# Optimization experiments

Hardware: AMD Instinct MI355X
Metric: run time of the kernel (lower is better)

The kernel has to match this reference:

```python
import jax, jax.numpy as jnp
import numpy as np

D = 128; PATCH = 16; NE = 1024; BETA = 0.25; EPS = 1e-5

def _conv1d(x, w, b, stride=1, pad=(0, 0)):
    # x: [N, Cin, L], w: [Cout, Cin, K] (torch OIW layout)
    x = jnp.pad(x, ((0, 0), (0, 0), pad))
    y = jax.lax.conv_general_dilated(x, w, (stride,), 'VALID', dimension_numbers=('NCH', 'OIH', 'NCH'))
    return y + b[None, :, None]

def _causal(x, w, b):
    # Conv1d(padding=k-1) followed by Chomp1d(k-1) == left-pad-only causal conv
    return _conv1d(x, w, b, pad=(w.shape[-1] - 1, 0))

def _block(x, w1, b1, w2, b2, wd=None, bd=None):
    h = jax.nn.relu(_causal(x, w1, b1))
    h = jax.nn.relu(_causal(h, w2, b2))
    res = x if wd is None else _conv1d(x, wd, bd)
    return jax.nn.relu(h + res)

def _forward(x, revin_w, revin_b, tb0_w1, tb0_b1, tb0_w2, tb0_b2, tb0_wd, tb0_bd,
             tb1_w1, tb1_b1, tb1_w2, tb1_b2, proj_w, proj_b, embed,
             up_w, up_b, dec_w1, dec_b1, dec_w2, dec_b2):
    B, L, C = x.shape
    # channel-independent: [B, L, C] -> [B*C, L, 1]
    x = jnp.transpose(x, (0, 2, 1)).reshape(B * C, L, 1)
    # RevIN normalization over the time axis (affine, enc_in=1)
    mu = x.mean(axis=1, keepdims=True)
    var = x.var(axis=1, keepdims=True)
    x_norm = (x - mu) / jnp.sqrt(var + EPS) * revin_w + revin_b
    # TCN encoder on [B*C, 1, L]
    h = jnp.transpose(x_norm, (0, 2, 1))
    h = _block(h, tb0_w1, tb0_b1, tb0_w2, tb0_b2, tb0_wd, tb0_bd)
    h = _block(h, tb1_w1, tb1_b1, tb1_w2, tb1_b2)            # [B*C, D, L]
    # patchify: Conv1d(D, D, kernel=patch_len, stride=patch_len)
    pf = _conv1d(h, proj_w, proj_b, stride=PATCH)            # [B*C, D, P]
    pf = jnp.transpose(pf, (0, 2, 1))                        # [B*C, P, D]
    # Vector quantization (eval mode: no EMA buffer update)
    flat = pf.reshape(-1, D)                                 # [N, D]
    dist = (flat * flat).sum(1, keepdims=True) - 2.0 * (flat @ embed) + (embed * embed).sum(0, keepdims=True)
    ind = jnp.argmin(dist, axis=1)                           # [N]
    q = jnp.take(embed.T, ind, axis=0).reshape(pf.shape)     # [B*C, P, D]
    vq_loss = jnp.mean((jax.lax.stop_gradient(q) - pf) ** 2) * BETA
    z_q = pf + jax.lax.stop_gradient(q - pf)                 # straight-through
    # lightweight decoder: ConvTranspose1d(k=stride=patch_len) == per-patch expansion
    z = jnp.transpose(z_q, (0, 2, 1))                        # [B*C, D, P]
    up = jnp.einsum('bep,edj->bdpj', z, up_w).reshape(z.shape[0], up_w.shape[1], -1) + up_b[None, :, None]
    d = jax.nn.gelu(_conv1d(up, dec_w1, dec_b1, pad=(1, 1)), approximate=False)
    d = _conv1d(d, dec_w2, dec_b2, pad=(1, 1))
    dec_out = jnp.transpose(d, (0, 2, 1))                    # [B*C, L, 1]
    recon_loss = jnp.mean((dec_out - x_norm) ** 2)
    return z_q, recon_loss + vq_loss

def setup_inputs():
    key = jax.random.key(0)
    ks = jax.random.split(key, 24)
    n = lambda i, s: jax.random.normal(ks[i], s, jnp.float32)
    return {
        'x': n(0, (64, 1024, 8)),
        'revin_w': jnp.ones((1,), jnp.float32), 'revin_b': jnp.zeros((1,), jnp.float32),
        'tb0_w1': n(1, (D, 1, 3)) * 0.01, 'tb0_b1': n(2, (D,)) * 0.01,
        'tb0_w2': n(3, (D, D, 3)) * 0.01, 'tb0_b2': n(4, (D,)) * 0.01,
        'tb0_wd': n(5, (D, 1, 1)) * 0.01, 'tb0_bd': n(6, (D,)) * 0.01,
        'tb1_w1': n(7, (D, D, 3)) * 0.01, 'tb1_b1': n(8, (D,)) * 0.01,
        'tb1_w2': n(9, (D, D, 3)) * 0.01, 'tb1_b2': n(10, (D,)) * 0.01,
        'proj_w': n(11, (D, D, PATCH)) * 0.02, 'proj_b': n(12, (D,)) * 0.02,
        'embed': n(13, (D, NE)),
        'up_w': n(14, (D, D, PATCH)) * 0.02, 'up_b': n(15, (D,)) * 0.02,
        'dec_w1': n(16, (D // 2, D, 3)) * 0.05, 'dec_b1': n(17, (D // 2,)) * 0.05,
        'dec_w2': n(18, (1, D // 2, 3)) * 0.05, 'dec_b2': n(19, (1,)) * 0.05,
    }

def reference(x, revin_w, revin_b, tb0_w1, tb0_b1, tb0_w2, tb0_b2, tb0_wd, tb0_bd,
              tb1_w1, tb1_b1, tb1_w2, tb1_b2, proj_w, proj_b, embed,
              up_w, up_b, dec_w1, dec_b1, dec_w2, dec_b2):
    return _forward(x, revin_w, revin_b, tb0_w1, tb0_b1, tb0_w2, tb0_b2, tb0_wd, tb0_bd,
                    tb1_w1, tb1_b1, tb1_w2, tb1_b2, proj_w, proj_b, embed,
                    up_w, up_b, dec_w1, dec_b1, dec_w2, dec_b2)
```

## Files before the change

### kernel.cpp

```cpp
#include <hip/hip_runtime.h>

constexpr size_t OFF_XN  = 0;
constexpr size_t OFF_PF  = 524288;
constexpr size_t OFF_W2A = OFF_PF  + 4194304;
constexpr size_t OFF_W1B = OFF_W2A + 49152;
constexpr size_t OFF_W2B = OFF_W1B + 49152;
constexpr size_t OFF_PW  = OFF_W2B + 49152;
constexpr size_t OFF_UPW = OFF_PW  + 262144;
constexpr size_t OFF_W1D = OFF_UPW + 262144;
constexpr size_t OFF_EMT = OFF_W1D + 24576;
constexpr size_t OFF_EN  = OFF_EMT + 131072;
constexpr size_t OFF_RP  = OFF_EN  + 1024;
constexpr size_t OFF_VP  = OFF_RP  + 8192;
constexpr size_t OFF_IND = OFF_VP  + 4096;

#define DI __device__ __forceinline__

__global__ __launch_bounds__(256) void k_prep(
    const float* __restrict__ w2a, const float* __restrict__ w1b, const float* __restrict__ w2b,
    const float* __restrict__ pw,  const float* __restrict__ upw, const float* __restrict__ w1d,
    const float* __restrict__ em,  float* __restrict__ ws)
{
  int tid = blockIdx.x * 256 + threadIdx.x;
  int stride = gridDim.x * 256;
  for (int i = tid; i < 128*128*3; i += stride) {
    int d = i / 384, r = i % 384;
    ws[OFF_W2A + (size_t)r*128 + d] = w2a[i];
    ws[OFF_W1B + (size_t)r*128 + d] = w1b[i];
    ws[OFF_W2B + (size_t)r*128 + d] = w2b[i];
  }
  for (int i = tid; i < 128*128*16; i += stride) {
    int d = i / 2048, r = i % 2048;
    ws[OFF_PW + (size_t)r*128 + d] = pw[i];
  }
  for (int i = tid; i < 128*128*16; i += stride) {
    int e = i / 2048, rem = i % 2048;
    int d = rem / 16, j = rem % 16;
    ws[OFF_UPW + (size_t)(j*128 + e)*128 + d] = upw[i];
  }
  for (int i = tid; i < 64*128*3; i += stride) {
    int o = i / 384, r = i % 384;
    ws[OFF_W1D + (size_t)r*64 + o] = w1d[i];
  }
  for (int j = tid; j < 1024; j += stride) {
    float s = 0.f;
    for (int d = 0; d < 128; ++d) {
      float v = em[d*1024 + j];
      ws[OFF_EMT + (size_t)j*128 + d] = v;
      s = fmaf(v, v, s);
    }
    ws[OFF_EN + j] = s;
  }
}

__global__ __launch_bounds__(256) void k_revin(
    const float* __restrict__ x, const float* __restrict__ rw, const float* __restrict__ rb,
    float* __restrict__ xn)
{
  int n = blockIdx.x;
  int b = n >> 3, c = n & 7;
  int t = threadIdx.x;
  const float* xp = x + (size_t)b*8192 + c;
  float v[4]; float s = 0.f, s2 = 0.f;
  #pragma unroll
  for (int i = 0; i < 4; ++i) {
    v[i] = xp[(size_t)(t + i*256)*8];
    s += v[i]; s2 = fmaf(v[i], v[i], s2);
  }
  __shared__ float sh[8];
  __shared__ float st[2];
  for (int o = 32; o; o >>= 1) { s += __shfl_down(s, o, 64); s2 += __shfl_down(s2, o, 64); }
  if ((t & 63) == 0) { sh[t >> 6] = s; sh[4 + (t >> 6)] = s2; }
  __syncthreads();
  if (t == 0) {
    float S = sh[0]+sh[1]+sh[2]+sh[3];
    float S2 = sh[4]+sh[5]+sh[6]+sh[7];
    float mu = S * (1.f/1024.f);
    float var = S2 * (1.f/1024.f) - mu*mu;
    st[0] = mu;
    st[1] = 1.f / sqrtf(var + 1e-5f);
  }
  __syncthreads();
  float mu = st[0], inv = st[1], w0 = rw[0], b0 = rb[0];
  #pragma unroll
  for (int i = 0; i < 4; ++i)
    xn[(size_t)n*1024 + t + i*256] = fmaf((v[i]-mu)*inv, w0, b0);
}

constexpr int STA = 70;
constexpr int STB = 68;

__global__ __launch_bounds__(512) void k_enc(
    const float* __restrict__ xn, float* __restrict__ pf,
    const float* __restrict__ w1a, const float* __restrict__ b1a,
    const float* __restrict__ w2aT, const float* __restrict__ b2a,
    const float* __restrict__ wd,  const float* __restrict__ bd,
    const float* __restrict__ w1bT, const float* __restrict__ b1b,
    const float* __restrict__ w2bT, const float* __restrict__ b2b,
    const float* __restrict__ pwT, const float* __restrict__ pb)
{
  __shared__ float xs[72];
  __shared__ __align__(16) float bufA[64*STA];
  __shared__ __align__(16) float bufB[128*STB];
  int n = blockIdx.x >> 4, tile = blockIdx.x & 15;
  int l0 = tile * 64;
  int t = threadIdx.x;
  int lane = t & 63;
  int w = __builtin_amdgcn_readfirstlane(t >> 6);
  int d0 = w * 16;

  if (t < 72) {
    int gl = l0 - 8 + t;
    xs[t] = (gl >= 0) ? xn[(size_t)n*1024 + gl] : 0.f;
  }
  __syncthreads();

  float acc2[16];
  #pragma unroll
  for (int i = 0; i < 16; ++i) acc2[i] = 0.f;
  float hacc[4] = {0.f, 0.f, 0.f, 0.f};

  for (int rep = 0; rep < 2; ++rep) {
    {
      int row = t & 63, colg = t >> 6;
      int c = rep*64 + row;
      float w0 = w1a[c*3+0], w1 = w1a[c*3+1], w2 = w1a[c*3+2], bb = b1a[c];
      #pragma unroll
      for (int i = 0; i < 9; ++i) {
        int j = colg*9 + i;
        if (j < 70) {
          float v = fmaf(w0, xs[j], fmaf(w1, xs[j+1], fmaf(w2, xs[j+2], bb)));
          bufA[row*STA + j] = (l0 - 6 + j >= 0) ? fmaxf(v, 0.f) : 0.f;
        }
      }
    }
    __syncthreads();
    for (int cc2 = 0; cc2 < 64; ++cc2) {
      float r0 = bufA[cc2*STA + lane + 4];
      float r1 = bufA[cc2*STA + lane + 5];
      float r2 = bufA[cc2*STA + lane + 6];
      const float4* wp = (const float4*)(w2aT + (size_t)(rep*64 + cc2)*384 + d0);
      #pragma unroll
      for (int jj = 0; jj < 4; ++jj) {
        float4 a = wp[jj], b = wp[32+jj], c4 = wp[64+jj];
        acc2[jj*4+0] = fmaf(a.x, r0, fmaf(b.x, r1, fmaf(c4.x, r2, acc2[jj*4+0])));
        acc2[jj*4+1] = fmaf(a.y, r0, fmaf(b.y, r1, fmaf(c4.y, r2, acc2[jj*4+1])));
        acc2[jj*4+2] = fmaf(a.z, r0, fmaf(b.z, r1, fmaf(c4.z, r2, acc2[jj*4+2])));
        acc2[jj*4+3] = fmaf(a.w, r0, fmaf(b.w, r1, fmaf(c4.w, r2, acc2[jj*4+3])));
      }
    }
    if (t < 128) {
      for (int cc2 = 0; cc2 < 64; ++cc2) {
        const float* wp = w2aT + (size_t)(rep*64 + cc2)*384 + t;
        float w0 = wp[0], w1 = wp[128], w2 = wp[256];
        float q0 = bufA[cc2*STA+0], q1 = bufA[cc2*STA+1], q2 = bufA[cc2*STA+2],
              q3 = bufA[cc2*STA+3], q4 = bufA[cc2*STA+4], q5 = bufA[cc2*STA+5];
        hacc[0] = fmaf(w0, q0, fmaf(w1, q1, fmaf(w2, q2, hacc[0])));
        hacc[1] = fmaf(w0, q1, fmaf(w1, q2, fmaf(w2, q3, hacc[1])));
        hacc[2] = fmaf(w0, q2, fmaf(w1, q3, fmaf(w2, q4, hacc[2])));
        hacc[3] = fmaf(w0, q3, fmaf(w1, q4, fmaf(w2, q5, hacc[3])));
      }
    }
    __syncthreads();
  }

  {
    float xv = xs[lane + 8];
    #pragma unroll
    for (int i = 0; i < 16; ++i) {
      int d = d0 + i;
      bufB[d*STB + lane + 4] =
        fmaxf(fmaxf(acc2[i] + b2a[d], 0.f) + fmaf(wd[d], xv, bd[d]), 0.f);
    }
    if (t < 128) {
      #pragma unroll
      for (int h = 0; h < 4; ++h) {
        int l = l0 - 4 + h;
        float o = 0.f;
        if (l >= 0)
          o = fmaxf(fmaxf(hacc[h] + b2a[t], 0.f) + fmaf(wd[t], xs[h+4], bd[t]), 0.f);
        bufB[t*STB + h] = o;
      }
    }
  }
  __syncthreads();

  float acc4[16];
  #pragma unroll
  for (int i = 0; i < 16; ++i) acc4[i] = 0.f;
  for (int rep = 0; rep < 2; ++rep) {
    {
      float acc3[8];
      #pragma unroll
      for (int i = 0; i < 8; ++i) acc3[i] = 0.f;
      int dh = rep*64 + w*8;
      for (int cc = 0; cc < 128; ++cc) {
        float r0 = bufB[cc*STB + lane];
        float r1 = bufB[cc*STB + lane + 1];
        float r2 = bufB[cc*STB + lane + 2];
        const float4* wp = (const float4*)(w1bT + (size_t)cc*384 + dh);
        float4 a0 = wp[0],  a1 = wp[1];
        float4 b0 = wp[32], b1 = wp[33];
        float4 c0 = wp[64], c1 = wp[65];
        acc3[0] = fmaf(a0.x, r0, fmaf(b0.x, r1, fmaf(c0.x, r2, acc3[0])));
        acc3[1] = fmaf(a0.y, r0, fmaf(b0.y, r1, fmaf(c0.y, r2, acc3[1])));
        acc3[2] = fmaf(a0.z, r0, fmaf(b0.z, r1, fmaf(c0.z, r2, acc3[2])));
        acc3[3] = fmaf(a0.w, r0, fmaf(b0.w, r1, fmaf(c0.w, r2, acc3[3])));
        acc3[4] = fmaf(a1.x, r0, fmaf(b1.x, r1, fmaf(c1.x, r2, acc3[4])));
        acc3[5] = fmaf(a1.y, r0, fmaf(b1.y, r1, fmaf(c1.y, r2, acc3[5])));
        acc3[6] = fmaf(a1.z, r0, fmaf(b1.z, r1, fmaf(c1.z, r2, acc3[6])));
        acc3[7] = fmaf(a1.w, r0, fmaf(b1.w, r1, fmaf(c1.w, r2, acc3[7])));
      }
      bool valid = (l0 - 2 + lane >= 0);
      #pragma unroll
      for (int i = 0; i < 8; ++i)
        bufA[(w*8+i)*STA + lane] = valid ? fmaxf(acc3[i] + b1b[dh+i], 0.f) : 0.f;
      if (t < 64) {
        int d = rep*64 + t;
        float h0 = 0.f, h1v = 0.f;
        for (int cc = 0; cc < 128; ++cc) {
          const float* wp = w1bT + (size_t)cc*384 + d;
          float w0 = wp[0], w1 = wp[128], w2 = wp[256];
          float q0 = bufB[cc*STB + 64], q1 = bufB[cc*STB + 65],
                q2 = bufB[cc*STB + 66], q3 = bufB[cc*STB + 67];
          h0  = fmaf(w0, q0, fmaf(w1, q1, fmaf(w2, q2, h0)));
          h1v = fmaf(w0, q1, fmaf(w1, q2, fmaf(w2, q3, h1v)));
        }
        bufA[t*STA + 64] = fmaxf(h0  + b1b[d], 0.f);
        bufA[t*STA + 65] = fmaxf(h1v + b1b[d], 0.f);
      }
    }
    __syncthreads();
    for (int row = 0; row < 64; ++row) {
      float r0 = bufA[row*STA + lane];
      float r1 = bufA[row*STA + lane + 1];
      float r2 = bufA[row*STA + lane + 2];
      const float4* wp = (const float4*)(w2bT + (size_t)(rep*64 + row)*384 + d0);
      #pragma unroll
      for (int jj = 0; jj < 4; ++jj) {
        float4 a = wp[jj], b = wp[32+jj], c4 = wp[64+jj];
        acc4[jj*4+0] = fmaf(a.x, r0, fmaf(b.x, r1, fmaf(c4.x, r2, acc4[jj*4+0])));
        acc4[jj*4+1] = fmaf(a.y, r0, fmaf(b.y, r1, fmaf(c4.y, r2, acc4[jj*4+1])));
        acc4[jj*4+2] = fmaf(a.z, r0, fmaf(b.z, r1, fmaf(c4.z, r2, acc4[jj*4+2])));
        acc4[jj*4+3] = fmaf(a.w, r0, fmaf(b.w, r1, fmaf(c4.w, r2, acc4[jj*4+3])));
      }
    }
    __syncthreads();
  }

  {
    float o1[16];
    #pragma unroll
    for (int i = 0; i < 16; ++i) {
      float res = bufB[(d0+i)*STB + lane + 4];
      o1[i] = fmaxf(fmaxf(acc4[i] + b2b[d0+i], 0.f) + res, 0.f);
    }
    __syncthreads();
    #pragma unroll
    for (int i = 0; i < 16; ++i) bufB[(d0+i)*STB + lane] = o1[i];
  }
  __syncthreads();

  {
    int cq = t >> 7, dd = t & 127;
    float accp[4] = {0.f, 0.f, 0.f, 0.f};
    for (int cl = 0; cl < 32; ++cl) {
      int c = cq*32 + cl;
      const float* row = bufB + c*STB;
      const float* wrow = pwT + (size_t)c*2048 + dd;
      float wv[16];
      #pragma unroll
      for (int k = 0; k < 16; ++k) wv[k] = wrow[(size_t)k*128];
      #pragma unroll
      for (int p = 0; p < 4; ++p) {
        float4 a0 = *(const float4*)(row + p*16);
        float4 a1 = *(const float4*)(row + p*16 + 4);
        float4 a2 = *(const float4*)(row + p*16 + 8);
        float4 a3 = *(const float4*)(row + p*16 + 12);
        accp[p] = fmaf(a0.x, wv[0],  accp[p]);
        accp[p] = fmaf(a0.y, wv[1],  accp[p]);
        accp[p] = fmaf(a0.z, wv[2],  accp[p]);
        accp[p] = fmaf(a0.w, wv[3],  accp[p]);
        accp[p] = fmaf(a1.x, wv[4],  accp[p]);
        accp[p] = fmaf(a1.y, wv[5],  accp[p]);
        accp[p] = fmaf(a1.z, wv[6],  accp[p]);
        accp[p] = fmaf(a1.w, wv[7],  accp[p]);
        accp[p] = fmaf(a2.x, wv[8],  accp[p]);
        accp[p] = fmaf(a2.y, wv[9],  accp[p]);
        accp[p] = fmaf(a2.z, wv[10], accp[p]);
        accp[p] = fmaf(a2.w, wv[11], accp[p]);
        accp[p] = fmaf(a3.x, wv[12], accp[p]);
        accp[p] = fmaf(a3.y, wv[13], accp[p]);
        accp[p] = fmaf(a3.z, wv[14], accp[p]);
        accp[p] = fmaf(a3.w, wv[15], accp[p]);
      }
    }
    #pragma unroll
    for (int p = 0; p < 4; ++p) bufA[(cq*4 + p)*128 + dd] = accp[p];
  }
  __syncthreads();
  {
    int p = t >> 7, dd = t & 127;
    float s = bufA[p*128 + dd];
    s += bufA[(4 + p)*128 + dd];
    s += bufA[(8 + p)*128 + dd];
    s += bufA[(12 + p)*128 + dd];
    pf[((size_t)n*64 + tile*4 + p)*128 + dd] = s + pb[dd];
  }
}

__global__ __launch_bounds__(256) void k_vq(float* ws)
{
  __shared__ __align__(16) float fT[128*132];
  __shared__ __align__(16) float ech[64*128];
  __shared__ float ens[64];
  __shared__ float2 red[128*16];
  const float* pf  = ws + OFF_PF;
  const float* emT = ws + OFF_EMT;
  const float* en  = ws + OFF_EN;
  int* ind = (int*)(ws + OFF_IND);

  int t = threadIdx.x;
  int r0 = blockIdx.x * 128;
  for (int s = t; s < 16384; s += 256) {
    int rr = s >> 7, d = s & 127;
    fT[d*132 + rr] = pf[(size_t)(r0 + rr)*128 + d];
  }
  int rg = t & 15, jg = t >> 4;
  float bv[8]; int bi[8];
  #pragma unroll
  for (int r = 0; r < 8; ++r) { bv[r] = 3.4e38f; bi[r] = 0; }

  for (int ch = 0; ch < 16; ++ch) {
    __syncthreads();
    {
      const float4* src = (const float4*)(emT + (size_t)ch*8192);
      for (int q = t; q < 2048; q += 256) {
        int jj = q >> 5, dq4 = q & 31;
        *(float4*)(ech + jj*128 + ((dq4*4) ^ ((jj&7)<<2))) = src[q];
      }
      if (t < 64) ens[t] = en[ch*64 + t];
    }
    __syncthreads();
    float acc[8][4] = {};
    for (int db = 0; db < 128; db += 4) {
      float4 e0 = *(const float4*)(ech + (jg*4+0)*128 + (db ^ (((jg*4+0)&7)<<2)));
      float4 e1 = *(const float4*)(ech + (jg*4+1)*128 + (db ^ (((jg*4+1)&7)<<2)));
      float4 e2 = *(const float4*)(ech + (jg*4+2)*128 + (db ^ (((jg*4+2)&7)<<2)));
      float4 e3 = *(const float4*)(ech + (jg*4+3)*128 + (db ^ (((jg*4+3)&7)<<2)));
      #pragma unroll
      for (int u = 0; u < 4; ++u) {
        const float* fp = fT + (db+u)*132 + rg*8;
        float4 fa = *(const float4*)fp;
        float4 fb = *(const float4*)(fp + 4);
        float fv[8] = {fa.x,fa.y,fa.z,fa.w,fb.x,fb.y,fb.z,fb.w};
        float ev[4] = { ((const float*)&e0)[u], ((const float*)&e1)[u],
                        ((const float*)&e2)[u], ((const float*)&e3)[u] };
        #pragma unroll
        for (int r = 0; r < 8; ++r)
          #pragma unroll
          for (int j = 0; j < 4; ++j)
            acc[r][j] = fmaf(fv[r], ev[j], acc[r][j]);
      }
    }
    #pragma unroll
    for (int r = 0; r < 8; ++r)
      #pragma unroll
      for (int j = 0; j < 4; ++j) {
        float dist = ens[jg*4 + j] - 2.f*acc[r][j];
        int code = ch*64 + jg*4 + j;
        if (dist < bv[r]) { bv[r] = dist; bi[r] = code; }
      }
  }
  __syncthreads();
  #pragma unroll
  for (int r = 0; r < 8; ++r)
    red[(rg*8 + r)*16 + jg] = make_float2(bv[r], __int_as_float(bi[r]));
  __syncthreads();
  if (t < 128) {
    float2 v0 = red[t*16 + 0];
    float best = v0.x; int besti = __float_as_int(v0.y);
    for (int j = 1; j < 16; ++j) {
      float2 v = red[t*16 + j];
      int vi = __float_as_int(v.y);
      if (v.x < best || (v.x == best && vi < besti)) { best = v.x; besti = vi; }
    }
    ind[r0 + t] = besti;
  }
}

__global__ __launch_bounds__(256) void k_gather(float* ws, float* __restrict__ dout)
{
  const float* pf  = ws + OFF_PF;
  const float* emT = ws + OFF_EMT;
  const int* ind = (const int*)(ws + OFF_IND);
  float* vq_part = ws + OFF_VP;

  int t = threadIdx.x;
  int d = t & 127;
  float s = 0.f;
  #pragma unroll
  for (int it = 0; it < 4; ++it) {
    int rr = (t >> 7) + it*2;
    size_t row = (size_t)blockIdx.x*8 + rr;
    int idx = ind[row];
    float q = emT[(size_t)idx*128 + d];
    float f = pf[row*128 + d];
    float qm = q - f;
    dout[row*128 + d] = f + qm;
    s = fmaf(qm, qm, s);
  }
  __shared__ float sh[4];
  for (int o = 32; o; o >>= 1) s += __shfl_down(s, o, 64);
  if ((t & 63) == 0) sh[t >> 6] = s;
  __syncthreads();
  if (t == 0) vq_part[blockIdx.x] = sh[0]+sh[1]+sh[2]+sh[3];
}

DI float gelu_f(float x) {
  float u = x * fmaf(0.0356774081f, x*x, 0.7978845608f);
  float e = __expf(2.f * u);
  float th = 1.f - 2.f / (e + 1.f);
  return 0.5f * x * (1.f + th);
}

__global__ __launch_bounds__(512) void k_decoder(
    const float* __restrict__ zq, float* ws,
    const float* __restrict__ upb, const float* __restrict__ db1,
    const float* __restrict__ dw2, const float* __restrict__ db2)
{
  constexpr int UPS = 70;
  constexpr int DS  = 70;
  __shared__ __align__(16) float ztT[128*8];
  __shared__ __align__(16) float up_s[128*UPS];
  __shared__ __align__(16) float dsh[64*DS];
  __shared__ __align__(16) float wd2[200];

  const float* upwT = ws + OFF_UPW;
  const float* w1dT = ws + OFF_W1D;
  const float* xn   = ws + OFF_XN;
  float* recon_part = ws + OFF_RP;

  int blk = blockIdx.x;
  int n = blk >> 4, tile = blk & 15;
  int l0 = tile*64, p0 = tile*4;
  int t = threadIdx.x;
  int lane = t & 63;
  int w = __builtin_amdgcn_readfirstlane(t >> 6);

  for (int s = t; s < 768; s += 512) {
    int e = s & 127, pi = s >> 7;
    int p = p0 - 1 + pi;
    ztT[e*8 + pi] = (p >= 0 && p < 64) ? zq[((size_t)n*64 + p)*128 + e] : 0.f;
  }
  __syncthreads();

  {
    int jj = t >> 5;
    int d4 = (t & 31) * 4;
    float acc[6][4] = {};
    const float* wbase = upwT + (size_t)jj*16384 + d4;
    for (int e = 0; e < 128; ++e) {
      float4 z0 = *(const float4*)(ztT + e*8);
      float2 z1 = *(const float2*)(ztT + e*8 + 4);
      float zr[6] = {z0.x, z0.y, z0.z, z0.w, z1.x, z1.y};
      float4 wv = *(const float4*)(wbase + (size_t)e*128);
      #pragma unroll
      for (int pi = 0; pi < 6; ++pi) {
        acc[pi][0] = fmaf(zr[pi], wv.x, acc[pi][0]);
        acc[pi][1] = fmaf(zr[pi], wv.y, acc[pi][1]);
        acc[pi][2] = fmaf(zr[pi], wv.z, acc[pi][2]);
        acc[pi][3] = fmaf(zr[pi], wv.w, acc[pi][3]);
      }
    }
    float ub0 = upb[d4], ub1 = upb[d4+1], ub2 = upb[d4+2], ub3 = upb[d4+3];
    #pragma unroll
    for (int pi = 0; pi < 6; ++pi) {
      int l = (p0 - 1 + pi)*16 + jj;
      int col = l - l0 + 2;
      if (col >= 0 && col < 68) {
        bool v = ((unsigned)l < 1024u);
        up_s[(d4+0)*UPS + col] = v ? acc[pi][0] + ub0 : 0.f;
        up_s[(d4+1)*UPS + col] = v ? acc[pi][1] + ub1 : 0.f;
        up_s[(d4+2)*UPS + col] = v ? acc[pi][2] + ub2 : 0.f;
        up_s[(d4+3)*UPS + col] = v ? acc[pi][3] + ub3 : 0.f;
      }
    }
  }
  __syncthreads();

  {
    int o0 = w * 8;
    float accd[8];
    #pragma unroll
    for (int i = 0; i < 8; ++i) accd[i] = 0.f;
    for (int c = 0; c < 128; ++c) {
      float r0 = up_s[c*UPS + lane];
      float r1 = up_s[c*UPS + lane + 1];
      float r2 = up_s[c*UPS + lane + 2];
      const float* wb = w1dT + (size_t)c*192 + o0;
      float4 wa0 = *(const float4*)(wb);
      float4 wa1 = *(const float4*)(wb + 4);
      float4 wb0 = *(const float4*)(wb + 64);
      float4 wb1 = *(const float4*)(wb + 68);
      float4 wc0 = *(const float4*)(wb + 128);
      float4 wc1 = *(const float4*)(wb + 132);
      accd[0] = fmaf(wa0.x, r0, fmaf(wb0.x, r1, fmaf(wc0.x, r2, accd[0])));
      accd[1] = fmaf(wa0.y, r0, fmaf(wb0.y, r1, fmaf(wc0.y, r2, accd[1])));
      accd[2] = fmaf(wa0.z, r0, fmaf(wb0.z, r1, fmaf(wc0.z, r2, accd[2])));
      accd[3] = fmaf(wa0.w, r0, fmaf(wb0.w, r1, fmaf(wc0.w, r2, accd[3])));
      accd[4] = fmaf(wa1.x, r0, fmaf(wb1.x, r1, fmaf(wc1.x, r2, accd[4])));
      accd[5] = fmaf(wa1.y, r0, fmaf(wb1.y, r1, fmaf(wc1.y, r2, accd[5])));
      accd[6] = fmaf(wa1.z, r0, fmaf(wb1.z, r1, fmaf(wc1.z, r2, accd[6])));
      accd[7] = fmaf(wa1.w, r0, fmaf(wb1.w, r1, fmaf(wc1.w, r2, accd[7])));
    }
    float hv = 0.f;
    int ho = t & 63, hc = 64 + (t >> 6);
    if (t < 128) {
      for (int c = 0; c < 128; ++c) {
        float q0 = up_s[c*UPS + hc];
        float q1 = up_s[c*UPS + hc + 1];
        float q2 = up_s[c*UPS + hc + 2];
        const float* wb = w1dT + (size_t)c*192 + ho;
        hv = fmaf(wb[0], q0, fmaf(wb[64], q1, fmaf(wb[128], q2, hv)));
      }
    }
    {
      int l = l0 - 1 + lane;
      bool v = ((unsigned)l < 1024u);
      #pragma unroll
      for (int i = 0; i < 8; ++i) {
        float x = accd[i] + db1[o0+i];
        dsh[(o0+i)*DS + lane] = v ? gelu_f(x) : 0.f;
      }
    }
    if (t < 128) {
      int l = l0 - 1 + hc;
      bool v = ((unsigned)l < 1024u);
      float x = hv + db1[ho];
      dsh[ho*DS + hc] = v ? gelu_f(x) : 0.f;
    }
  }
  if (t < 192) wd2[t] = dw2[t];
  __syncthreads();

  if (t < 256) {
    int loff = t & 63, ch = t >> 6;
    float part = 0.f;
    for (int cl = 0; cl < 16; ++cl) {
      int c = ch*16 + cl;
      part = fmaf(wd2[c*3+0], dsh[c*DS + loff],
             fmaf(wd2[c*3+1], dsh[c*DS + loff + 1],
             fmaf(wd2[c*3+2], dsh[c*DS + loff + 2], part)));
    }
    ztT[loff*4 + ch] = part;
  }
  __syncthreads();
  if (t < 64) {
    float acc = ztT[t*4+0] + ztT[t*4+1] + ztT[t*4+2] + ztT[t*4+3] + db2[0];
    float diff = acc - xn[(size_t)n*1024 + l0 + t];
    float part = diff*diff;
    for (int o = 32; o; o >>= 1) part += __shfl_down(part, o, 64);
    if (t == 0) recon_part[blk] = part;
  }
}

__global__ __launch_bounds__(256) void k_finalize(const float* __restrict__ ws, float* __restrict__ dout)
{
  const float* rp = ws + OFF_RP;
  const float* vp = ws + OFF_VP;
  int t = threadIdx.x;
  float s1 = 0.f, s2 = 0.f;
  for (int i = t; i < 8192; i += 256) s1 += rp[i];
  for (int i = t; i < 4096; i += 256) s2 += vp[i];
  __shared__ float sh[8];
  for (int o = 32; o; o >>= 1) { s1 += __shfl_down(s1,o,64); s2 += __shfl_down(s2,o,64); }
  if ((t & 63) == 0) { sh[t >> 6] = s1; sh[4 + (t >> 6)] = s2; }
  __syncthreads();
  if (t == 0) {
    float R = sh[0]+sh[1]+sh[2]+sh[3];
    float V = sh[4]+sh[5]+sh[6]+sh[7];
    dout[4194304] = R * (1.f/524288.f) + 0.25f * (V * (1.f/4194304.f));
  }
}

extern "C" void kernel_launch(void* const* d_in, const int* in_sizes, int n_in,
                              void* d_out, int out_size, void* d_ws, size_t ws_size,
                              hipStream_t stream)
{
  const float* x    = (const float*)d_in[0];
  const float* rw   = (const float*)d_in[1];
  const float* rb   = (const float*)d_in[2];
  const float* w1a  = (const float*)d_in[3];
  const float* b1a  = (const float*)d_in[4];
  const float* w2a  = (const float*)d_in[5];
  const float* b2a  = (const float*)d_in[6];
  const float* wda  = (const float*)d_in[7];
  const float* bda  = (const float*)d_in[8];
  const float* w1b  = (const float*)d_in[9];
  const float* b1b  = (const float*)d_in[10];
  const float* w2b  = (const float*)d_in[11];
  const float* b2b  = (const float*)d_in[12];
  const float* pw   = (const float*)d_in[13];
  const float* pb   = (const float*)d_in[14];
  const float* em   = (const float*)d_in[15];
  const float* upw  = (const float*)d_in[16];
  const float* upb  = (const float*)d_in[17];
  const float* dw1  = (const float*)d_in[18];
  const float* db1  = (const float*)d_in[19];
  const float* dw2  = (const float*)d_in[20];
  const float* db2  = (const float*)d_in[21];
  float* ws = (float*)d_ws;
  float* out = (float*)d_out;

  float* xn = ws + OFF_XN;
  float* pf = ws + OFF_PF;
  const float* w2aT = ws + OFF_W2A;
  const float* w1bT = ws + OFF_W1B;
  const float* w2bT = ws + OFF_W2B;
  const float* pwT  = ws + OFF_PW;

  k_prep<<<256, 256, 0, stream>>>(w2a, w1b, w2b, pw, upw, dw1, em, ws);
  k_revin<<<512, 256, 0, stream>>>(x, rw, rb, xn);
  k_enc<<<8192, 512, 0, stream>>>(xn, pf, w1a, b1a, w2aT, b2a, wda, bda,
                                  w1bT, b1b, w2bT, b2b, pwT, pb);
  k_vq<<<256, 256, 0, stream>>>(ws);
  k_gather<<<4096, 256, 0, stream>>>(ws, out);
  k_decoder<<<8192, 512, 0, stream>>>(out, ws, upb, db1, dw2, db2);
  k_finalize<<<1, 256, 0, stream>>>(ws, out);
}
```

Measured before the change: 3.243 ms.

## Restructure tb1 conv stage to single pass and rework patch projection tiling

Replaces the two-rep split of the second TCN block's first conv with a single pass in which each thread computes 16 output channels, storing the intermediate back into bufB. The conv2 stage then runs once over all 128 rows, and the residual is kept in registers instead of being re-read from shared memory. The patch projection is retiled into 8 channel groups with float2 weight loads per thread, and the final reduction sums 8 partials. This cuts the redundant halo computation and extra barriers, but increases register pressure and the number of partial sums.

```diff
diff --git a/kernel.cpp b/kernel.cpp
--- a/kernel.cpp
+++ b/kernel.cpp
@@ -164,13 +164,15 @@
     __syncthreads();
   }
 
+  float res[16];
   {
     float xv = xs[lane + 8];
     #pragma unroll
     for (int i = 0; i < 16; ++i) {
       int d = d0 + i;
-      bufB[d*STB + lane + 4] =
-        fmaxf(fmaxf(acc2[i] + b2a[d], 0.f) + fmaf(wd[d], xv, bd[d]), 0.f);
+      float o = fmaxf(fmaxf(acc2[i] + b2a[d], 0.f) + fmaf(wd[d], xv, bd[d]), 0.f);
+      res[i] = o;
+      bufB[d*STB + lane + 4] = o;
     }
     if (t < 128) {
       #pragma unroll
@@ -185,126 +187,107 @@
   }
   __syncthreads();
 
-  float acc4[16];
-  #pragma unroll
-  for (int i = 0; i < 16; ++i) acc4[i] = 0.f;
-  for (int rep = 0; rep < 2; ++rep) {
-    {
-      float acc3[8];
-      #pragma unroll
-      for (int i = 0; i < 8; ++i) acc3[i] = 0.f;
-      int dh = rep*64 + w*8;
-      for (int cc = 0; cc < 128; ++cc) {
-        float r0 = bufB[cc*STB + lane];
-        float r1 = bufB[cc*STB + lane + 1];
-        float r2 = bufB[cc*STB + lane + 2];
-        const float4* wp = (const float4*)(w1bT + (size_t)cc*384 + dh);
-        float4 a0 = wp[0],  a1 = wp[1];
-        float4 b0 = wp[32], b1 = wp[33];
-        float4 c0 = wp[64], c1 = wp[65];
-        acc3[0] = fmaf(a0.x, r0, fmaf(b0.x, r1, fmaf(c0.x, r2, acc3[0])));
-        acc3[1] = fmaf(a0.y, r0, fmaf(b0.y, r1, fmaf(c0.y, r2, acc3[1])));
-        acc3[2] = fmaf(a0.z, r0, fmaf(b0.z, r1, fmaf(c0.z, r2, acc3[2])));
-        acc3[3] = fmaf(a0.w, r0, fmaf(b0.w, r1, fmaf(c0.w, r2, acc3[3])));
-        acc3[4] = fmaf(a1.x, r0, fmaf(b1.x, r1, fmaf(c1.x, r2, acc3[4])));
-        acc3[5] = fmaf(a1.y, r0, fmaf(b1.y, r1, fmaf(c1.y, r2, acc3[5])));
-        acc3[6] = fmaf(a1.z, r0, fmaf(b1.z, r1, fmaf(c1.z, r2, acc3[6])));
-        acc3[7] = fmaf(a1.w, r0, fmaf(b1.w, r1, fmaf(c1.w, r2, acc3[7])));
-      }
-      bool valid = (l0 - 2 + lane >= 0);
-      #pragma unroll
-      for (int i = 0; i < 8; ++i)
-        bufA[(w*8+i)*STA + lane] = valid ? fmaxf(acc3[i] + b1b[dh+i], 0.f) : 0.f;
-      if (t < 64) {
-        int d = rep*64 + t;
-        float h0 = 0.f, h1v = 0.f;
-        for (int cc = 0; cc < 128; ++cc) {
-          const float* wp = w1bT + (size_t)cc*384 + d;
-          float w0 = wp[0], w1 = wp[128], w2 = wp[256];
-          float q0 = bufB[cc*STB + 64], q1 = bufB[cc*STB + 65],
-                q2 = bufB[cc*STB + 66], q3 = bufB[cc*STB + 67];
-          h0  = fmaf(w0, q0, fmaf(w1, q1, fmaf(w2, q2, h0)));
-          h1v = fmaf(w0, q1, fmaf(w1, q2, fmaf(w2, q3, h1v)));
-        }
-        bufA[t*STA + 64] = fmaxf(h0  + b1b[d], 0.f);
-        bufA[t*STA + 65] = fmaxf(h1v + b1b[d], 0.f);
-      }
-    }
-    __syncthreads();
-    for (int row = 0; row < 64; ++row) {
-      float r0 = bufA[row*STA + lane];
-      float r1 = bufA[row*STA + lane + 1];
-      float r2 = bufA[row*STA + lane + 2];
-      const float4* wp = (const float4*)(w2bT + (size_t)(rep*64 + row)*384 + d0);
+  {
+    float acc3[16];
+    #pragma unroll
+    for (int i = 0; i < 16; ++i) acc3[i] = 0.f;
+    for (int cc = 0; cc < 128; ++cc) {
+      float r0 = bufB[cc*STB + lane];
+      float r1 = bufB[cc*STB + lane + 1];
+      float r2 = bufB[cc*STB + lane + 2];
+      const float4* wp = (const float4*)(w1bT + (size_t)cc*384 + d0);
       #pragma unroll
       for (int jj = 0; jj < 4; ++jj) {
         float4 a = wp[jj], b = wp[32+jj], c4 = wp[64+jj];
-        acc4[jj*4+0] = fmaf(a.x, r0, fmaf(b.x, r1, fmaf(c4.x, r2, acc4[jj*4+0])));
-        acc4[jj*4+1] = fmaf(a.y, r0, fmaf(b.y, r1, fmaf(c4.y, r2, acc4[jj*4+1])));
-        acc4[jj*4+2] = fmaf(a.z, r0, fmaf(b.z, r1, fmaf(c4.z, r2, acc4[jj*4+2])));
-        acc4[jj*4+3] = fmaf(a.w, r0, fmaf(b.w, r1, fmaf(c4.w, r2, acc4[jj*4+3])));
+        acc3[jj*4+0] = fmaf(a.x, r0, fmaf(b.x, r1, fmaf(c4.x, r2, acc3[jj*4+0])));
+        acc3[jj*4+1] = fmaf(a.y, r0, fmaf(b.y, r1, fmaf(c4.y, r2, acc3[jj*4+1])));
+        acc3[jj*4+2] = fmaf(a.z, r0, fmaf(b.z, r1, fmaf(c4.z, r2, acc3[jj*4+2])));
+        acc3[jj*4+3] = fmaf(a.w, r0, fmaf(b.w, r1, fmaf(c4.w, r2, acc3[jj*4+3])));
+      }
+    }
+    float haccb = 0.f;
+    int hrow = t & 127, hc = 64 + (t >> 7);
+    if (t < 256) {
+      for (int cc = 0; cc < 128; ++cc) {
+        float q0 = bufB[cc*STB + hc];
+        float q1 = bufB[cc*STB + hc + 1];
+        float q2 = bufB[cc*STB + hc + 2];
+        const float* wp = w1bT + (size_t)cc*384 + hrow;
+        haccb = fmaf(wp[0], q0, fmaf(wp[128], q1, fmaf(wp[256], q2, haccb)));
       }
     }
     __syncthreads();
-  }
+    {
+      bool valid = (l0 - 2 + lane >= 0);
+      #pragma unroll
+      for (int i = 0; i < 16; ++i)
+        bufB[(d0+i)*STB + lane] = valid ? fmaxf(acc3[i] + b1b[d0+i], 0.f) : 0.f;
+      if (t < 256)
+        bufB[hrow*STB + hc] = fmaxf(haccb + b1b[hrow], 0.f);
+    }
+  }
+  __syncthreads();
+
+  float acc4[16];
+  #pragma unroll
+  for (int i = 0; i < 16; ++i) acc4[i] = 0.f;
+  for (int row = 0; row < 128; ++row) {
+    float r0 = bufB[row*STB + lane];
+    float r1 = bufB[row*STB + lane + 1];
+    float r2 = bufB[row*STB + lane + 2];
+    const float4* wp = (const float4*)(w2bT + (size_t)row*384 + d0);
+    #pragma unroll
+    for (int jj = 0; jj < 4; ++jj) {
+      float4 a = wp[jj], b = wp[32+jj], c4 = wp[64+jj];
+      acc4[jj*4+0] = fmaf(a.x, r0, fmaf(b.x, r1, fmaf(c4.x, r2, acc4[jj*4+0])));
+      acc4[jj*4+1] = fmaf(a.y, r0, fmaf(b.y, r1, fmaf(c4.y, r2, acc4[jj*4+1])));
+      acc4[jj*4+2] = fmaf(a.z, r0, fmaf(b.z, r1, fmaf(c4.z, r2, acc4[jj*4+2])));
+      acc4[jj*4+3] = fmaf(a.w, r0, fmaf(b.w, r1, fmaf(c4.w, r2, acc4[jj*4+3])));
+    }
+  }
+  __syncthreads();
+  #pragma unroll
+  for (int i = 0; i < 16; ++i)
+    bufB[(d0+i)*STB + lane] = fmaxf(fmaxf(acc4[i] + b2b[d0+i], 0.f) + res[i], 0.f);
+  __syncthreads();
 
   {
-    float o1[16];
-    #pragma unroll
-    for (int i = 0; i < 16; ++i) {
-      float res = bufB[(d0+i)*STB + lane + 4];
-      o1[i] = fmaxf(fmaxf(acc4[i] + b2b[d0+i], 0.f) + res, 0.f);
-    }
-    __syncthreads();
-    #pragma unroll
-    for (int i = 0; i < 16; ++i) bufB[(d0+i)*STB + lane] = o1[i];
-  }
-  __syncthreads();
-
-  {
-    int cq = t >> 7, dd = t & 127;
-    float accp[4] = {0.f, 0.f, 0.f, 0.f};
-    for (int cl = 0; cl < 32; ++cl) {
-      int c = cq*32 + cl;
+    int cq = t >> 6, ddp = t & 63;
+    float acc[4][2] = {};
+    for (int cl = 0; cl < 16; ++cl) {
+      int c = cq*16 + cl;
       const float* row = bufB + c*STB;
-      const float* wrow = pwT + (size_t)c*2048 + dd;
-      float wv[16];
-      #pragma unroll
-      for (int k = 0; k < 16; ++k) wv[k] = wrow[(size_t)k*128];
-      #pragma unroll
-      for (int p = 0; p < 4; ++p) {
-        float4 a0 = *(const float4*)(row + p*16);
-        float4 a1 = *(const float4*)(row + p*16 + 4);
-        float4 a2 = *(const float4*)(row + p*16 + 8);
-        float4 a3 = *(const float4*)(row + p*16 + 12);
-        accp[p] = fmaf(a0.x, wv[0],  accp[p]);
-        accp[p] = fmaf(a0.y, wv[1],  accp[p]);
-        accp[p] = fmaf(a0.z, wv[2],  accp[p]);
-        accp[p] = fmaf(a0.w, wv[3],  accp[p]);
-        accp[p] = fmaf(a1.x, wv[4],  accp[p]);
-        accp[p] = fmaf(a1.y, wv[5],  accp[p]);
-        accp[p] = fmaf(a1.z, wv[6],  accp[p]);
-        accp[p] = fmaf(a1.w, wv[7],  accp[p]);
-        accp[p] = fmaf(a2.x, wv[8],  accp[p]);
-        accp[p] = fmaf(a2.y, wv[9],  accp[p]);
-        accp[p] = fmaf(a2.z, wv[10], accp[p]);
-        accp[p] = fmaf(a2.w, wv[11], accp[p]);
-        accp[p] = fmaf(a3.x, wv[12], accp[p]);
-        accp[p] = fmaf(a3.y, wv[13], accp[p]);
-        accp[p] = fmaf(a3.z, wv[14], accp[p]);
-        accp[p] = fmaf(a3.w, wv[15], accp[p]);
-      }
-    }
-    #pragma unroll
-    for (int p = 0; p < 4; ++p) bufA[(cq*4 + p)*128 + dd] = accp[p];
+      const float* wbase = pwT + (size_t)c*2048 + 2*ddp;
+      #pragma unroll
+      for (int k4 = 0; k4 < 4; ++k4) {
+        float2 wv0 = *(const float2*)(wbase + (size_t)(k4*4+0)*128);
+        float2 wv1 = *(const float2*)(wbase + (size_t)(k4*4+1)*128);
+        float2 wv2 = *(const float2*)(wbase + (size_t)(k4*4+2)*128);
+        float2 wv3 = *(const float2*)(wbase + (size_t)(k4*4+3)*128);
+        #pragma unroll
+        for (int p = 0; p < 4; ++p) {
+          float4 av = *(const float4*)(row + p*16 + k4*4);
+          acc[p][0] = fmaf(av.x, wv0.x, acc[p][0]);
+          acc[p][1] = fmaf(av.x, wv0.y, acc[p][1]);
+          acc[p][0] = fmaf(av.y, wv1.x, acc[p][0]);
+          acc[p][1] = fmaf(av.y, wv1.y, acc[p][1]);
+          acc[p][0] = fmaf(av.z, wv2.x, acc[p][0]);
+          acc[p][1] = fmaf(av.z, wv2.y, acc[p][1]);
+          acc[p][0] = fmaf(av.w, wv3.x, acc[p][0]);
+          acc[p][1] = fmaf(av.w, wv3.y, acc[p][1]);
+        }
+      }
+    }
+    #pragma unroll
+    for (int p = 0; p < 4; ++p)
+      *(float2*)(bufA + (cq*4 + p)*128 + 2*ddp) = make_float2(acc[p][0], acc[p][1]);
   }
   __syncthreads();
   {
     int p = t >> 7, dd = t & 127;
-    float s = bufA[p*128 + dd];
-    s += bufA[(4 + p)*128 + dd];
-    s += bufA[(8 + p)*128 + dd];
-    s += bufA[(12 + p)*128 + dd];
+    float s = 0.f;
+    #pragma unroll
+    for (int cq = 0; cq < 8; ++cq) s += bufA[(cq*4 + p)*128 + dd];
     pf[((size_t)n*64 + tile*4 + p)*128 + dd] = s + pb[dd];
   }
 }
```

Measured after the change: 4.084 ms. +25.9%, slower.
